# Optimization experiments

Hardware: AMD Instinct MI355X
Metric: run time of the kernel (lower is better)

## Reference

```python
import jax, jax.numpy as jnp
import numpy as np

N, K, SD, ID, ZD, ED, H, FC, AT, FT = 10000, 31, 8, 2, 32, 64, 128, 128, 16, 6
DT = 0.25


def setup_inputs() -> dict:
    key = jax.random.key(0)
    ks = iter(jax.random.split(key, 48))

    def p(shape, s=0.08):
        return (s * jax.random.normal(next(ks), shape)).astype(jnp.float32)

    E = N * K
    inp = {
        'state_history': p([4, N, SD], 1.0),          # only last slice is used
        'z': p([N, ZD], 1.0),                         # latent code per node
        'edge_idx1': jnp.repeat(jnp.arange(N), K),    # owning node of each edge
        'edge_idx2': jax.random.randint(next(ks), [E], 0, N),  # neighbor node
        'node_obs_idx': 1 + jnp.arange(E).reshape(N, K),  # +1: row 0 of enc table is the zero-pad row
        'W_edge': p([2 * SD, ED]), 'b_edge': jnp.zeros([ED], jnp.float32),
        'att_W1': p([ED, AT]), 'att_W2': p([SD, AT]), 'att_v': p([AT]),
        'obs_Wi': p([ED, 4 * H]), 'obs_Wh': p([H, 4 * H]), 'obs_b': jnp.zeros([4 * H], jnp.float32),
        'st_Wi': p([SD + ID, 4 * H]), 'st_Wh': p([H, 4 * H]), 'st_b': jnp.zeros([4 * H], jnp.float32),
        'oh0_W': p([SD, H]), 'oh0_b': jnp.zeros([H], jnp.float32),
        'oc0_W': p([SD, H]), 'oc0_b': jnp.zeros([H], jnp.float32),
        'sh0_W': p([SD, H]), 'sh0_b': jnp.zeros([H], jnp.float32),
        'sc0_W': p([SD, H]), 'sc0_b': jnp.zeros([H], jnp.float32),
        'act_W1': p([SD + H + H + ZD, FC]), 'act_b1': jnp.zeros([FC], jnp.float32),
        'act_W2': p([FC, ID]), 'act_b2': jnp.zeros([ID], jnp.float32),
        'dyn_A': p([SD, SD]), 'dyn_B': p([SD, ID]),
        'ft': FT,
    }
    return inp


def _lstm_step(x, h, c, Wi, Wh, b):
    g = x @ Wi + h @ Wh + b
    i, f, gg, o = jnp.split(g, 4, axis=-1)  # torch gate order i,f,g,o
    c2 = jax.nn.sigmoid(f) * c + jax.nn.sigmoid(i) * jnp.tanh(gg)
    h2 = jax.nn.sigmoid(o) * jnp.tanh(c2)
    return h2, c2


def reference(state_history, z, edge_idx1, edge_idx2, node_obs_idx,
              W_edge, b_edge, att_W1, att_W2, att_v,
              obs_Wi, obs_Wh, obs_b, st_Wi, st_Wh, st_b,
              oh0_W, oh0_b, oc0_W, oc0_b, sh0_W, sh0_b, sc0_W, sc0_b,
              act_W1, act_b1, act_W2, act_b2, dyn_A, dyn_B, ft):
    s0 = state_history[-1]                      # [N, SD]
    oh = s0 @ oh0_W + oh0_b                     # LSTM initial states from last history state
    oc = s0 @ oc0_W + oc0_b
    sh = s0 @ sh0_W + sh0_b
    sc = s0 @ sc0_W + sc0_b
    u0 = jnp.zeros((s0.shape[0], dyn_B.shape[1]), s0.dtype)

    def step(carry, _):
        s, u, oh, oc, sh, sc = carry
        # heterogeneous edge encoding: gather endpoint states, encode
        e = jnp.concatenate([s[edge_idx1], s[edge_idx2]], axis=-1)   # [E, 2*SD]
        enc = jax.nn.relu(e @ W_edge + b_edge)                       # [E, ED]
        enc_pad = jnp.concatenate([jnp.zeros((1, enc.shape[1]), enc.dtype), enc], axis=0)
        obs = enc_pad[node_obs_idx]                                  # [N, K, ED] gather
        rel = s - s0                                                  # rel_state_fun
        # additive attention over each node's K observed edges
        score = jnp.einsum('nki,i->nk', jnp.tanh(obs @ att_W1 + (rel @ att_W2)[:, None, :]), att_v)
        alpha = jax.nn.softmax(score, axis=-1)
        ctx = jnp.einsum('nk,nke->ne', alpha, obs)                   # [N, ED]
        oh2, oc2 = _lstm_step(ctx, oh, oc, obs_Wi, obs_Wh, obs_b)
        sh2, sc2 = _lstm_step(jnp.concatenate([rel, u], axis=-1), sh, sc, st_Wi, st_Wh, st_b)
        a = jnp.concatenate([rel, oh2, sh2, z], axis=-1)             # [N, SD+2H+ZD]
        u2 = jax.nn.relu(a @ act_W1 + act_b1) @ act_W2 + act_b2      # action net (input_scale=1)
        s2 = s + DT * (s @ dyn_A.T + u2 @ dyn_B.T)                   # dyn_net rollout
        return (s2, u2, oh2, oc2, sh2, sc2), (s2, u2)

    _, (state_pred, input_pred) = jax.lax.scan(step, (s0, u0, oh, oc, sh, sc), None, length=ft)
    return state_pred, input_pred  # [ft, N, SD], [ft, N, ID]
```

## Files before the change

kernel.cpp:

```cpp
#include <hip/hip_runtime.h>
#include <hip/hip_bf16.h>
#include <math.h>

#define N_NODES 10000
#define KE 31
#define SD 8
#define ID 2
#define ZD 32
#define ED 64
#define HH 128
#define FC 128
#define AT 16
#define FT 6
#define DT_C 0.25f
#define NB 4

#define NTU 20
#define MT 2

#define NKS_O 6
#define NKS_S 5
#define NKS_A 10

#define WP_OBS_SZ 49152
#define WP_ST_SZ  40960
#define WP_ACT_SZ 20480
#define WP_EDGE_SZ 1024
#define WP_ATT1_SZ 512

typedef __bf16 bf16x8 __attribute__((ext_vector_type(8)));
typedef float  f32x4  __attribute__((ext_vector_type(4)));

__device__ __forceinline__ float sigm(float x){ return 1.0f/(1.0f+exp2f(-1.44269504f*x)); }
__device__ __forceinline__ float tanh_f(float x){ return 1.0f - 2.0f/(1.0f+exp2f(2.88539008f*x)); }

__device__ __forceinline__ unsigned short f2b(float f){
  __hip_bfloat16 h = __float2bfloat16(f);
  return __builtin_bit_cast(unsigned short, h);
}
__device__ __forceinline__ float b2f(unsigned short x){
  unsigned int u = ((unsigned int)x) << 16;
  return __builtin_bit_cast(float, u);
}
__device__ __forceinline__ unsigned int pack2(float a, float b){
  return (unsigned int)f2b(a) | ((unsigned int)f2b(b) << 16);
}
__device__ __forceinline__ bf16x8 as_bf16x8(int4 v){
  union { int4 i; bf16x8 b; } u; u.i = v; return u.b;
}
__device__ __forceinline__ int hwaddr(int e, int d){
  return e*64 + ((((d>>3)<<3) ^ ((e&7)<<3)) + (d&7));
}

__global__ __launch_bounds__(256) void pack_weights(
    const float* __restrict__ obs_Wi, const float* __restrict__ obs_Wh,
    const float* __restrict__ st_Wi,  const float* __restrict__ st_Wh,
    const float* __restrict__ act_W1, const float* __restrict__ W_edge,
    const float* __restrict__ att_W1,
    unsigned int* __restrict__ wp_obs, unsigned int* __restrict__ wp_st,
    unsigned int* __restrict__ wp_act, unsigned int* __restrict__ wp_edge,
    unsigned int* __restrict__ wp_att1)
{
  int t = blockIdx.x*256 + threadIdx.x;
  if (t < 49152){
    int c = t / 1536; int r = t - c*1536;
    int ks = r >> 8; int q = r & 255;
    int ln = q >> 2; int dw = q & 3;
    int k  = ks*32 + ((ln>>4)<<3) + dw*2;
    int col = (c<<4) + (ln & 15);
    float v0 = (k   < 64) ? obs_Wi[k*4*HH + col]      : obs_Wh[(k-64)*4*HH + col];
    float v1 = (k+1 < 64) ? obs_Wi[(k+1)*4*HH + col]  : obs_Wh[(k-63)*4*HH + col];
    wp_obs[t] = pack2(v0, v1);
  } else if (t < 90112){
    int t2 = t - 49152;
    int c = t2 / 1280; int r = t2 - c*1280;
    int ks = r >> 8; int q = r & 255;
    int ln = q >> 2; int dw = q & 3;
    int k  = ks*32 + ((ln>>4)<<3) + dw*2;
    int col = (c<<4) + (ln & 15);
    float v0, v1;
    { int kk=k;   v0 = (kk<10)? st_Wi[kk*4*HH+col] : (kk<138 ? st_Wh[(kk-10)*4*HH+col] : 0.f); }
    { int kk=k+1; v1 = (kk<10)? st_Wi[kk*4*HH+col] : (kk<138 ? st_Wh[(kk-10)*4*HH+col] : 0.f); }
    wp_st[t2] = pack2(v0, v1);
  } else if (t < 110592){
    int t3 = t - 90112;
    int c = t3 / 2560; int r = t3 - c*2560;
    int ks = r >> 8; int q = r & 255;
    int ln = q >> 2; int dw = q & 3;
    int k  = ks*32 + ((ln>>4)<<3) + dw*2;
    int col = (c<<4) + (ln & 15);
    float v0 = (k   < 296) ? act_W1[k*FC + col]     : 0.f;
    float v1 = (k+1 < 296) ? act_W1[(k+1)*FC + col] : 0.f;
    wp_act[t3] = pack2(v0, v1);
  } else if (t < 111616){
    int t4 = t - 110592;
    int c = t4 >> 8; int r = t4 & 255;
    int ln = r >> 2; int dw = r & 3;
    int k  = ((ln>>4)<<3) + dw*2;
    int col = (c<<4) + (ln & 15);
    float v0 = (k   < 16) ? W_edge[k*ED + col]     : 0.f;
    float v1 = (k+1 < 16) ? W_edge[(k+1)*ED + col] : 0.f;
    wp_edge[t4] = pack2(v0, v1);
  } else if (t < 112128){
    int t5 = t - 111616;
    int ks = t5 >> 8; int r = t5 & 255;
    int ln = r >> 2; int dw = r & 3;
    int k  = ks*32 + ((ln>>4)<<3) + dw*2;
    int col = ln & 15;
    float v0 = (k   < 64) ? att_W1[k*AT + col]     : 0.f;
    float v1 = (k+1 < 64) ? att_W1[(k+1)*AT + col] : 0.f;
    wp_att1[t5] = pack2(v0, v1);
  }
}

__global__ __launch_bounds__(256) void init_kernel(
    const float* __restrict__ s0,
    const float* __restrict__ oh0_W, const float* __restrict__ oh0_b,
    const float* __restrict__ oc0_W, const float* __restrict__ oc0_b,
    const float* __restrict__ sh0_W, const float* __restrict__ sh0_b,
    const float* __restrict__ sc0_W, const float* __restrict__ sc0_b,
    unsigned short* __restrict__ oh, unsigned short* __restrict__ oc,
    unsigned short* __restrict__ sh, unsigned short* __restrict__ sc,
    float* __restrict__ u, unsigned short* __restrict__ s0bf)
{
  int t = blockIdx.x*256 + threadIdx.x;
  if (t < N_NODES*ID) u[t] = 0.0f;
  if (t < N_NODES*SD) s0bf[t] = f2b(s0[t]);
  if (t >= N_NODES*HH) return;
  int n = t >> 7, j = t & 127;
  float s[SD];
  #pragma unroll
  for (int i=0;i<SD;i++) s[i] = s0[n*SD+i];
  float a0=oh0_b[j], a1=oc0_b[j], a2=sh0_b[j], a3=sc0_b[j];
  #pragma unroll
  for (int i=0;i<SD;i++){
    a0 = fmaf(s[i], oh0_W[i*HH+j], a0);
    a1 = fmaf(s[i], oc0_W[i*HH+j], a1);
    a2 = fmaf(s[i], sh0_W[i*HH+j], a2);
    a3 = fmaf(s[i], sc0_W[i*HH+j], a3);
  }
  oh[t]=f2b(a0); oc[t]=f2b(a1); sh[t]=f2b(a2); sc[t]=f2b(a3);
}

__global__ __launch_bounds__(256) void edge_att_mfma(
    const float* __restrict__ s_prev, const float* __restrict__ s0,
    const unsigned short* __restrict__ sprev_bf,
    const int* __restrict__ edge_idx1, const int* __restrict__ edge_idx2,
    const int* __restrict__ node_obs_idx,
    const unsigned int* __restrict__ wp_edge, const unsigned int* __restrict__ wp_att1,
    const float* __restrict__ b_edge, const float* __restrict__ att_W2,
    const float* __restrict__ att_v, unsigned short* __restrict__ ctx)
{
  __shared__ __align__(16) unsigned int eF[8*64*4];
  __shared__ __align__(16) unsigned short encL[128*64];
  __shared__ __align__(16) unsigned int pF[4*64*4];
  __shared__ float scores[128];
  __shared__ float relbuf[NB][SD];
  __shared__ float relW2b[NB][AT];
  __shared__ unsigned char emask[128];

  const int tid  = threadIdx.x;
  const int lane = tid & 63;
  const int w    = tid >> 6;
  const int n0   = blockIdx.x * NB;
  const int EPB  = NB*KE;

  {
    ((uint4*)pF)[tid] = (uint4){0,0,0,0};
    int eb  = tid >> 1;
    int khi = tid & 1;
    int valid = 0;
    uint4 d = (uint4){0,0,0,0};
    if (eb < EPB){
      int nl = eb / KE;
      int j  = eb - nl*KE;
      int idx = node_obs_idx[(n0+nl)*KE + j];
      if (idx > 0){
        valid = 1;
        int e = idx - 1;
        int i = khi ? edge_idx2[e] : edge_idx1[e];
        d = *(const uint4*)&sprev_bf[i*SD];
      }
    }
    int mt = eb >> 4;
    int base = ((mt<<6) + (eb&15) + (khi<<4)) << 2;
    ((uint4*)&eF[base])[0] = d;
    int zbase = ((mt<<6) + (eb&15) + ((khi+2)<<4)) << 2;
    ((uint4*)&eF[zbase])[0] = (uint4){0,0,0,0};
    if (khi == 0) emask[eb] = (unsigned char)valid;
    if (tid < NB*SD){
      int m = tid >> 3, i = tid & 7;
      relbuf[m][i] = s_prev[(n0+m)*SD + i] - s0[(n0+m)*SD + i];
    }
  }
  __syncthreads();

  if (tid < NB*AT){
    int m = tid >> 4, a = tid & 15;
    float acc = 0.f;
    #pragma unroll
    for (int i = 0; i < SD; ++i) acc = fmaf(relbuf[m][i], att_W2[i*AT + a], acc);
    relW2b[m][a] = acc;
  }
  {
    const int c = lane & 15, g = lane >> 4;
    #pragma unroll
    for (int q = 0; q < 2; ++q){
      int mt = w*2 + q;
      bf16x8 A = as_bf16x8(*(const int4*)&eF[((mt<<6) + lane) << 2]);
      f32x4 acc[4];
      #pragma unroll
      for (int ct = 0; ct < 4; ++ct){
        bf16x8 B = as_bf16x8(*(const int4*)&wp_edge[((ct<<6) + lane) << 2]);
        acc[ct] = (f32x4){0,0,0,0};
        acc[ct] = __builtin_amdgcn_mfma_f32_16x16x32_bf16(A, B, acc[ct], 0, 0, 0);
      }
      #pragma unroll
      for (int ct = 0; ct < 4; ++ct){
        int d = ct*16 + c;
        float bias = b_edge[d];
        #pragma unroll
        for (int r = 0; r < 4; ++r){
          int eb = mt*16 + g*4 + r;
          float v = acc[ct][r] + bias;
          v = emask[eb] ? fmaxf(v, 0.f) : 0.f;
          encL[hwaddr(eb, d)] = f2b(v);
        }
      }
    }
  }
  __syncthreads();

  {
    const int c = lane & 15, g = lane >> 4;
    const float av = att_v[c];
    #pragma unroll
    for (int q = 0; q < 2; ++q){
      int mt = w*2 + q;
      int row = mt*16 + c;
      f32x4 acc = (f32x4){0,0,0,0};
      #pragma unroll
      for (int ks = 0; ks < 2; ++ks){
        int hw = row*64 + (((ks*4 + g) << 3) ^ ((row&7) << 3));
        bf16x8 A = *(const bf16x8*)&encL[hw];
        bf16x8 B = as_bf16x8(*(const int4*)&wp_att1[((ks<<6) + lane) << 2]);
        acc = __builtin_amdgcn_mfma_f32_16x16x32_bf16(A, B, acc, 0, 0, 0);
      }
      #pragma unroll
      for (int r = 0; r < 4; ++r){
        int eb = mt*16 + g*4 + r;
        int nm = eb / KE; if (nm > NB-1) nm = NB-1;
        float sv = av * tanh_f(acc[r] + relW2b[nm][c]);
        #pragma unroll
        for (int off = 1; off < 16; off <<= 1) sv += __shfl_xor(sv, off);
        if (c == 0 && eb < EPB) scores[eb] = sv;
      }
    }
  }
  __syncthreads();

  {
    int m = w;
    float sc_ = (lane < KE) ? scores[m*KE + lane] : -INFINITY;
    float mx = sc_;
    #pragma unroll
    for (int off = 32; off; off >>= 1) mx = fmaxf(mx, __shfl_xor(mx, off));
    float p = (lane < KE) ? exp2f(1.44269504f*(sc_ - mx)) : 0.f;
    float sm = p;
    #pragma unroll
    for (int off = 32; off; off >>= 1) sm += __shfl_xor(sm, off);
    float alpha = p / sm;
    if (lane < KE){
      int k = m*KE + lane;
      int ks = k >> 5;
      int ln = m | (((k>>3)&3) << 4);
      ((unsigned short*)pF)[((ks<<6) + ln)*8 + (k&7)] = f2b(alpha);
    }
  }
  __syncthreads();

  {
    const int c = lane & 15, g = lane >> 4;
    const int d = w*16 + c;
    f32x4 acc = (f32x4){0,0,0,0};
    #pragma unroll
    for (int ks = 0; ks < 4; ++ks){
      bf16x8 A = as_bf16x8(*(const int4*)&pF[((ks<<6) + lane) << 2]);
      union { unsigned short u[8]; bf16x8 v; } bb;
      #pragma unroll
      for (int j = 0; j < 8; ++j){
        int e = ks*32 + g*8 + j;
        bb.u[j] = encL[hwaddr(e, d)];
      }
      acc = __builtin_amdgcn_mfma_f32_16x16x32_bf16(A, bb.v, acc, 0, 0, 0);
    }
    if (g == 0){
      #pragma unroll
      for (int r = 0; r < 4; ++r){
        ctx[(n0 + r)*ED + d] = f2b(acc[r]);
      }
    }
  }
}

__global__ __launch_bounds__(512) void node_update_mfma(
    const float* __restrict__ s_prev, const float* __restrict__ s0,
    const float* __restrict__ z, const unsigned short* __restrict__ ctx,
    const unsigned int* __restrict__ wp_obs, const unsigned int* __restrict__ wp_st,
    const unsigned int* __restrict__ wp_act,
    const float* __restrict__ obs_b, const float* __restrict__ st_b,
    const float* __restrict__ act_b1,
    const float* __restrict__ act_W2, const float* __restrict__ act_b2,
    const float* __restrict__ dyn_A, const float* __restrict__ dyn_B,
    unsigned short* __restrict__ oh, unsigned short* __restrict__ oc,
    unsigned short* __restrict__ sh, unsigned short* __restrict__ sc,
    float* __restrict__ u, float* __restrict__ s_next,
    unsigned short* __restrict__ snext_bf,
    float* __restrict__ out_state, float* __restrict__ out_input, int tstep)
{
  __shared__ __align__(16) union UB {
    struct { unsigned int X1[MT*NKS_O*64*4]; unsigned int X2[MT*NKS_S*64*4]; } x;
    float F[32][FC+4];
  } ubuf;
  __shared__ __align__(16) unsigned int fragX3[MT*NKS_A*64*4];
  __shared__ float sps[32][SD];
  __shared__ float u2p[32][ID][4];
  __shared__ float u2s[32][ID];

  const int tid  = threadIdx.x;
  const int n0   = blockIdx.x * NTU;
  const int w    = tid >> 6;
  const int lane = tid & 63;
  const int hcol = w*16 + (lane & 15);

  float ocv[MT][4], scv[MT][4];
  #pragma unroll
  for (int Mt = 0; Mt < MT; ++Mt){
    #pragma unroll
    for (int r = 0; r < 4; ++r){
      int m = Mt*16 + ((lane>>4)<<2) + r;
      int gn = n0 + m;
      ocv[Mt][r] = (m < NTU) ? b2f(oc[gn*HH + hcol]) : 0.f;
      scv[Mt][r] = (m < NTU) ? b2f(sc[gn*HH + hcol]) : 0.f;
    }
  }

  for (int idx = tid; idx < 32*96; idx += 512){
    int m = idx / 96, kp = idx - m*96; int k0 = kp*2; int gn = n0 + m;
    unsigned int d = 0;
    if (m < NTU){
      if (k0 < ED) d = *(const unsigned int*)&ctx[gn*ED + k0];
      else         d = *(const unsigned int*)&oh[gn*HH + k0 - ED];
    }
    int Mt = m >> 4;
    int ln = (m & 15) | (((k0>>3)&3)<<4);
    ubuf.x.X1[(((Mt*NKS_O + (k0>>5))*64 + ln)<<2) + ((k0&7)>>1)] = d;
  }
  for (int idx = tid; idx < 32*80; idx += 512){
    int m = idx / 80, kp = idx - m*80; int k0 = kp*2; int gn = n0 + m;
    unsigned int d = 0;
    if (m < NTU){
      if (k0 < 8)        d = pack2(s_prev[gn*SD+k0]-s0[gn*SD+k0], s_prev[gn*SD+k0+1]-s0[gn*SD+k0+1]);
      else if (k0 == 8)  d = pack2(u[gn*ID], u[gn*ID+1]);
      else if (k0 < 138) d = *(const unsigned int*)&sh[gn*HH + k0 - 10];
    }
    int Mt = m >> 4;
    int ln = (m & 15) | (((k0>>3)&3)<<4);
    ubuf.x.X2[(((Mt*NKS_S + (k0>>5))*64 + ln)<<2) + ((k0&7)>>1)] = d;
  }
  for (int idx = tid; idx < 32*32; idx += 512){
    int m = idx / 32, p = idx - m*32; int gn = n0 + m;
    int k0 = (p < 4) ? p*2 : 256 + p*2;
    float v0 = 0.f, v1 = 0.f;
    if (m < NTU){
      if (k0 < 8){ v0 = s_prev[gn*SD+k0]-s0[gn*SD+k0]; v1 = s_prev[gn*SD+k0+1]-s0[gn*SD+k0+1]; }
      else if (k0 < 296){ v0 = z[gn*ZD + k0-264]; v1 = z[gn*ZD + k0-263]; }
    }
    int Mt = m >> 4;
    int ln = (m & 15) | (((k0>>3)&3)<<4);
    fragX3[(((Mt*NKS_A + (k0>>5))*64 + ln)<<2) + ((k0&7)>>1)] = pack2(v0, v1);
  }
  if (tid < NTU*SD){
    int m = tid >> 3, i = tid & 7;
    sps[m][i] = s_prev[(n0+m)*SD + i];
  }
  __syncthreads();

  {
    f32x4 acc[MT][4];
    #pragma unroll
    for (int Mt = 0; Mt < MT; ++Mt)
      #pragma unroll
      for (int g = 0; g < 4; ++g){
        float b = obs_b[g*HH + hcol];
        acc[Mt][g] = (f32x4){b, b, b, b};
      }
    #pragma unroll
    for (int ks = 0; ks < NKS_O; ++ks){
      bf16x8 a[MT];
      #pragma unroll
      for (int Mt = 0; Mt < MT; ++Mt)
        a[Mt] = as_bf16x8(*(const int4*)&ubuf.x.X1[(((Mt*NKS_O + ks)*64 + lane)<<2)]);
      #pragma unroll
      for (int g = 0; g < 4; ++g){
        int c = w + 8*g;
        bf16x8 b = as_bf16x8(*(const int4*)&wp_obs[(((c*NKS_O + ks)*64 + lane)<<2)]);
        #pragma unroll
        for (int Mt = 0; Mt < MT; ++Mt)
          acc[Mt][g] = __builtin_amdgcn_mfma_f32_16x16x32_bf16(a[Mt], b, acc[Mt][g], 0, 0, 0);
      }
    }
    #pragma unroll
    for (int Mt = 0; Mt < MT; ++Mt){
      #pragma unroll
      for (int r = 0; r < 4; ++r){
        int m = Mt*16 + ((lane>>4)<<2) + r; int gn = n0 + m;
        float h2 = 0.f;
        if (m < NTU){
          float gi = acc[Mt][0][r], gf = acc[Mt][1][r], gg = acc[Mt][2][r], go = acc[Mt][3][r];
          float c2 = sigm(gf)*ocv[Mt][r] + sigm(gi)*tanh_f(gg);
          h2 = sigm(go)*tanh_f(c2);
          oc[gn*HH + hcol] = f2b(c2);
          oh[gn*HH + hcol] = f2b(h2);
        }
        int k = 8 + hcol;
        int ln = (m & 15) | (((k>>3)&3)<<4);
        ((unsigned short*)fragX3)[(((m>>4)*NKS_A + (k>>5))*64 + ln)*8 + (k&7)] = f2b(h2);
      }
    }
  }

  {
    f32x4 acc[MT][4];
    #pragma unroll
    for (int Mt = 0; Mt < MT; ++Mt)
      #pragma unroll
      for (int g = 0; g < 4; ++g){
        float b = st_b[g*HH + hcol];
        acc[Mt][g] = (f32x4){b, b, b, b};
      }
    #pragma unroll
    for (int ks = 0; ks < NKS_S; ++ks){
      bf16x8 a[MT];
      #pragma unroll
      for (int Mt = 0; Mt < MT; ++Mt)
        a[Mt] = as_bf16x8(*(const int4*)&ubuf.x.X2[(((Mt*NKS_S + ks)*64 + lane)<<2)]);
      #pragma unroll
      for (int g = 0; g < 4; ++g){
        int c = w + 8*g;
        bf16x8 b = as_bf16x8(*(const int4*)&wp_st[(((c*NKS_S + ks)*64 + lane)<<2)]);
        #pragma unroll
        for (int Mt = 0; Mt < MT; ++Mt)
          acc[Mt][g] = __builtin_amdgcn_mfma_f32_16x16x32_bf16(a[Mt], b, acc[Mt][g], 0, 0, 0);
      }
    }
    #pragma unroll
    for (int Mt = 0; Mt < MT; ++Mt){
      #pragma unroll
      for (int r = 0; r < 4; ++r){
        int m = Mt*16 + ((lane>>4)<<2) + r; int gn = n0 + m;
        float h2 = 0.f;
        if (m < NTU){
          float gi = acc[Mt][0][r], gf = acc[Mt][1][r], gg = acc[Mt][2][r], go = acc[Mt][3][r];
          float c2 = sigm(gf)*scv[Mt][r] + sigm(gi)*tanh_f(gg);
          h2 = sigm(go)*tanh_f(c2);
          sc[gn*HH + hcol] = f2b(c2);
          sh[gn*HH + hcol] = f2b(h2);
        }
        int k = 136 + hcol;
        int ln = (m & 15) | (((k>>3)&3)<<4);
        ((unsigned short*)fragX3)[(((m>>4)*NKS_A + (k>>5))*64 + ln)*8 + (k&7)] = f2b(h2);
      }
    }
  }
  __syncthreads();

  {
    float b1 = act_b1[hcol];
    f32x4 acc[MT];
    #pragma unroll
    for (int Mt = 0; Mt < MT; ++Mt) acc[Mt] = (f32x4){b1, b1, b1, b1};
    #pragma unroll
    for (int ks = 0; ks < NKS_A; ++ks){
      bf16x8 bb = as_bf16x8(*(const int4*)&wp_act[(((w*NKS_A + ks)*64 + lane)<<2)]);
      #pragma unroll
      for (int Mt = 0; Mt < MT; ++Mt){
        bf16x8 a = as_bf16x8(*(const int4*)&fragX3[(((Mt*NKS_A + ks)*64 + lane)<<2)]);
        acc[Mt] = __builtin_amdgcn_mfma_f32_16x16x32_bf16(a, bb, acc[Mt], 0, 0, 0);
      }
    }
    #pragma unroll
    for (int Mt = 0; Mt < MT; ++Mt){
      #pragma unroll
      for (int r = 0; r < 4; ++r){
        int m = Mt*16 + ((lane>>4)<<2) + r;
        ubuf.F[m][hcol] = fmaxf(acc[Mt][r], 0.f);
      }
    }
  }
  __syncthreads();

  if (tid < 32*ID*4){
    int m  = tid >> 3;
    int c  = (tid >> 2) & 1;
    int kq = tid & 3;
    float p = 0.f;
    #pragma unroll
    for (int i = 0; i < 32; ++i){
      int j = kq*32 + i;
      p = fmaf(ubuf.F[m][j], act_W2[j*ID + c], p);
    }
    u2p[m][c][kq] = p;
  }
  __syncthreads();
  if (tid < NTU*ID){
    int m = tid >> 1, c = tid & 1; int gn = n0 + m;
    float s = act_b2[c] + u2p[m][c][0] + u2p[m][c][1] + u2p[m][c][2] + u2p[m][c][3];
    u2s[m][c] = s;
    u[gn*ID + c] = s;
    out_input[tstep*N_NODES*ID + gn*ID + c] = s;
  }
  __syncthreads();

  if (tid < NTU*SD){
    int m = tid >> 3, d = tid & 7; int gn = n0 + m;
    float acc = 0.f;
    #pragma unroll
    for (int e = 0; e < SD; ++e) acc = fmaf(sps[m][e], dyn_A[d*SD+e], acc);
    #pragma unroll
    for (int c = 0; c < ID; ++c) acc = fmaf(u2s[m][c], dyn_B[d*ID+c], acc);
    float s2v = sps[m][d] + DT_C*acc;
    s_next[gn*SD+d] = s2v;
    snext_bf[gn*SD+d] = f2b(s2v);
    out_state[tstep*N_NODES*SD + gn*SD + d] = s2v;
  }
}

extern "C" void kernel_launch(void* const* d_in, const int* in_sizes, int n_in,
                              void* d_out, int out_size, void* d_ws, size_t ws_size,
                              hipStream_t stream)
{
  const float* state_history = (const float*)d_in[0];
  const float* z        = (const float*)d_in[1];
  const int*   edge_idx1 = (const int*)d_in[2];
  const int*   edge_idx2 = (const int*)d_in[3];
  const int*   node_obs_idx = (const int*)d_in[4];
  const float* W_edge  = (const float*)d_in[5];
  const float* b_edge  = (const float*)d_in[6];
  const float* att_W1  = (const float*)d_in[7];
  const float* att_W2  = (const float*)d_in[8];
  const float* att_v   = (const float*)d_in[9];
  const float* obs_Wi  = (const float*)d_in[10];
  const float* obs_Wh  = (const float*)d_in[11];
  const float* obs_b   = (const float*)d_in[12];
  const float* st_Wi   = (const float*)d_in[13];
  const float* st_Wh   = (const float*)d_in[14];
  const float* st_b    = (const float*)d_in[15];
  const float* oh0_W   = (const float*)d_in[16];
  const float* oh0_b   = (const float*)d_in[17];
  const float* oc0_W   = (const float*)d_in[18];
  const float* oc0_b   = (const float*)d_in[19];
  const float* sh0_W   = (const float*)d_in[20];
  const float* sh0_b   = (const float*)d_in[21];
  const float* sc0_W   = (const float*)d_in[22];
  const float* sc0_b   = (const float*)d_in[23];
  const float* act_W1  = (const float*)d_in[24];
  const float* act_b1  = (const float*)d_in[25];
  const float* act_W2  = (const float*)d_in[26];
  const float* act_b2  = (const float*)d_in[27];
  const float* dyn_A   = (const float*)d_in[28];
  const float* dyn_B   = (const float*)d_in[29];

  const float* s0 = state_history + 3*N_NODES*SD;

  float* wsf = (float*)d_ws;
  float* sbuf0 = wsf;
  float* sbuf1 = sbuf0 + N_NODES*SD;
  float* u     = sbuf1 + N_NODES*SD;
  unsigned short* oh    = (unsigned short*)(u + N_NODES*ID);
  unsigned short* oc    = oh + N_NODES*HH;
  unsigned short* sh    = oc + N_NODES*HH;
  unsigned short* sc    = sh + N_NODES*HH;
  unsigned short* ctx   = sc + N_NODES*HH;
  unsigned short* s0bf  = ctx + N_NODES*ED;
  unsigned short* sbf0  = s0bf + N_NODES*SD;
  unsigned short* sbf1  = sbf0 + N_NODES*SD;
  float* sbuf[2] = { sbuf0, sbuf1 };
  unsigned short* sbf[2] = { sbf0, sbf1 };

  unsigned int* wp_obs  = (unsigned int*)(sbf1 + N_NODES*SD);
  unsigned int* wp_st   = wp_obs + WP_OBS_SZ;
  unsigned int* wp_act  = wp_st  + WP_ST_SZ;
  unsigned int* wp_edge = wp_act + WP_ACT_SZ;
  unsigned int* wp_att1 = wp_edge + WP_EDGE_SZ;

  float* out_state = (float*)d_out;
  float* out_input = out_state + FT*N_NODES*SD;

  hipLaunchKernelGGL(pack_weights, dim3(438), dim3(256), 0, stream,
      obs_Wi, obs_Wh, st_Wi, st_Wh, act_W1, W_edge, att_W1,
      wp_obs, wp_st, wp_act, wp_edge, wp_att1);

  hipLaunchKernelGGL(init_kernel, dim3((N_NODES*HH+255)/256), dim3(256), 0, stream,
      s0, oh0_W, oh0_b, oc0_W, oc0_b, sh0_W, sh0_b, sc0_W, sc0_b, oh, oc, sh, sc, u, s0bf);

  for (int t = 0; t < FT; ++t){
    const float* s_prev = (t==0) ? s0 : sbuf[(t-1)&1];
    const unsigned short* sprev_bf = (t==0) ? s0bf : sbf[(t-1)&1];
    float* s_next = sbuf[t&1];
    unsigned short* snext_bf = sbf[t&1];
    hipLaunchKernelGGL(edge_att_mfma, dim3(N_NODES/NB), dim3(256), 0, stream,
        s_prev, s0, sprev_bf, edge_idx1, edge_idx2, node_obs_idx,
        wp_edge, wp_att1, b_edge, att_W2, att_v, ctx);
    hipLaunchKernelGGL(node_update_mfma, dim3(N_NODES/NTU), dim3(512), 0, stream,
        s_prev, s0, z, ctx,
        wp_obs, wp_st, wp_act,
        obs_b, st_b, act_b1, act_W2, act_b2, dyn_A, dyn_B,
        oh, oc, sh, sc, u, s_next, snext_bf, out_state, out_input, t);
  }
}
```

Baseline: 310.0 us.

## Fill full 32-row MFMA tiles per block and split row tiles across 16 waves

The node update kernel now assigns 32 real nodes per block instead of 20, so the two 16-row MFMA tiles carry no padding rows. It also doubles the block to 1024 threads, giving each wave a single row tile (Mth) and a column tile (ct), so the gate and action GEMMs are spread over twice as many waves. A tail guard (nreal) handles the last partial block. The goal is less wasted MFMA work on padding and more parallelism per block. The cost is fewer blocks, larger register and LDS pressure per block, and repeated weight fragment loads across the two row-tile waves.

Measured after the change: 358.9 us. 1.16x slower.

```diff
diff --git a/kernel.cpp b/kernel.cpp
--- a/kernel.cpp
+++ b/kernel.cpp
@@ -15,7 +15,7 @@
 #define DT_C 0.25f
 #define NB 4
 
-#define NTU 20
+#define NTU 32
 #define MT 2
 
 #define NKS_O 6
@@ -303,7 +303,7 @@
   }
 }
 
-__global__ __launch_bounds__(512) void node_update_mfma(
+__global__ __launch_bounds__(1024) void node_update_mfma(
     const float* __restrict__ s_prev, const float* __restrict__ s0,
     const float* __restrict__ z, const unsigned short* __restrict__ ctx,
     const unsigned int* __restrict__ wp_obs, const unsigned int* __restrict__ wp_st,
@@ -329,26 +329,26 @@
 
   const int tid  = threadIdx.x;
   const int n0   = blockIdx.x * NTU;
+  const int nreal= (N_NODES - n0 < NTU) ? (N_NODES - n0) : NTU;
   const int w    = tid >> 6;
+  const int ct   = w & 7;
+  const int Mth  = w >> 3;
   const int lane = tid & 63;
-  const int hcol = w*16 + (lane & 15);
-
-  float ocv[MT][4], scv[MT][4];
+  const int hcol = ct*16 + (lane & 15);
+
+  float ocv[4], scv[4];
   #pragma unroll
-  for (int Mt = 0; Mt < MT; ++Mt){
-    #pragma unroll
-    for (int r = 0; r < 4; ++r){
-      int m = Mt*16 + ((lane>>4)<<2) + r;
-      int gn = n0 + m;
-      ocv[Mt][r] = (m < NTU) ? b2f(oc[gn*HH + hcol]) : 0.f;
-      scv[Mt][r] = (m < NTU) ? b2f(sc[gn*HH + hcol]) : 0.f;
-    }
-  }
-
-  for (int idx = tid; idx < 32*96; idx += 512){
+  for (int r = 0; r < 4; ++r){
+    int m = Mth*16 + ((lane>>4)<<2) + r;
+    int gn = n0 + m;
+    ocv[r] = (m < nreal) ? b2f(oc[gn*HH + hcol]) : 0.f;
+    scv[r] = (m < nreal) ? b2f(sc[gn*HH + hcol]) : 0.f;
+  }
+
+  for (int idx = tid; idx < 32*96; idx += 1024){
     int m = idx / 96, kp = idx - m*96; int k0 = kp*2; int gn = n0 + m;
     unsigned int d = 0;
-    if (m < NTU){
+    if (m < nreal){
       if (k0 < ED) d = *(const unsigned int*)&ctx[gn*ED + k0];
       else         d = *(const unsigned int*)&oh[gn*HH + k0 - ED];
     }
@@ -356,10 +356,10 @@
     int ln = (m & 15) | (((k0>>3)&3)<<4);
     ubuf.x.X1[(((Mt*NKS_O + (k0>>5))*64 + ln)<<2) + ((k0&7)>>1)] = d;
   }
-  for (int idx = tid; idx < 32*80; idx += 512){
+  for (int idx = tid; idx < 32*80; idx += 1024){
     int m = idx / 80, kp = idx - m*80; int k0 = kp*2; int gn = n0 + m;
     unsigned int d = 0;
-    if (m < NTU){
+    if (m < nreal){
       if (k0 < 8)        d = pack2(s_prev[gn*SD+k0]-s0[gn*SD+k0], s_prev[gn*SD+k0+1]-s0[gn*SD+k0+1]);
       else if (k0 == 8)  d = pack2(u[gn*ID], u[gn*ID+1]);
       else if (k0 < 138) d = *(const unsigned int*)&sh[gn*HH + k0 - 10];
@@ -368,11 +368,11 @@
     int ln = (m & 15) | (((k0>>3)&3)<<4);
     ubuf.x.X2[(((Mt*NKS_S + (k0>>5))*64 + ln)<<2) + ((k0&7)>>1)] = d;
   }
-  for (int idx = tid; idx < 32*32; idx += 512){
+  for (int idx = tid; idx < 32*32; idx += 1024){
     int m = idx / 32, p = idx - m*32; int gn = n0 + m;
     int k0 = (p < 4) ? p*2 : 256 + p*2;
     float v0 = 0.f, v1 = 0.f;
-    if (m < NTU){
+    if (m < nreal){
       if (k0 < 8){ v0 = s_prev[gn*SD+k0]-s0[gn*SD+k0]; v1 = s_prev[gn*SD+k0+1]-s0[gn*SD+k0+1]; }
       else if (k0 < 296){ v0 = z[gn*ZD + k0-264]; v1 = z[gn*ZD + k0-263]; }
     }
@@ -382,120 +382,92 @@
   }
   if (tid < NTU*SD){
     int m = tid >> 3, i = tid & 7;
-    sps[m][i] = s_prev[(n0+m)*SD + i];
-  }
-  __syncthreads();
-
-  {
-    f32x4 acc[MT][4];
-    #pragma unroll
-    for (int Mt = 0; Mt < MT; ++Mt)
+    sps[m][i] = (m < nreal) ? s_prev[(n0+m)*SD + i] : 0.f;
+  }
+  __syncthreads();
+
+  {
+    f32x4 acc[4];
+    #pragma unroll
+    for (int g = 0; g < 4; ++g){
+      float b = obs_b[g*HH + hcol];
+      acc[g] = (f32x4){b, b, b, b};
+    }
+    #pragma unroll
+    for (int ks = 0; ks < NKS_O; ++ks){
+      bf16x8 a = as_bf16x8(*(const int4*)&ubuf.x.X1[(((Mth*NKS_O + ks)*64 + lane)<<2)]);
       #pragma unroll
       for (int g = 0; g < 4; ++g){
-        float b = obs_b[g*HH + hcol];
-        acc[Mt][g] = (f32x4){b, b, b, b};
-      }
-    #pragma unroll
-    for (int ks = 0; ks < NKS_O; ++ks){
-      bf16x8 a[MT];
-      #pragma unroll
-      for (int Mt = 0; Mt < MT; ++Mt)
-        a[Mt] = as_bf16x8(*(const int4*)&ubuf.x.X1[(((Mt*NKS_O + ks)*64 + lane)<<2)]);
+        int c = ct + 8*g;
+        bf16x8 b = as_bf16x8(*(const int4*)&wp_obs[(((c*NKS_O + ks)*64 + lane)<<2)]);
+        acc[g] = __builtin_amdgcn_mfma_f32_16x16x32_bf16(a, b, acc[g], 0, 0, 0);
+      }
+    }
+    #pragma unroll
+    for (int r = 0; r < 4; ++r){
+      int m = Mth*16 + ((lane>>4)<<2) + r; int gn = n0 + m;
+      float h2 = 0.f;
+      if (m < nreal){
+        float gi = acc[0][r], gf = acc[1][r], gg = acc[2][r], go = acc[3][r];
+        float c2 = sigm(gf)*ocv[r] + sigm(gi)*tanh_f(gg);
+        h2 = sigm(go)*tanh_f(c2);
+        oc[gn*HH + hcol] = f2b(c2);
+        oh[gn*HH + hcol] = f2b(h2);
+      }
+      int k = 8 + hcol;
+      int ln = (m & 15) | (((k>>3)&3)<<4);
+      ((unsigned short*)fragX3)[(((m>>4)*NKS_A + (k>>5))*64 + ln)*8 + (k&7)] = f2b(h2);
+    }
+  }
+
+  {
+    f32x4 acc[4];
+    #pragma unroll
+    for (int g = 0; g < 4; ++g){
+      float b = st_b[g*HH + hcol];
+      acc[g] = (f32x4){b, b, b, b};
+    }
+    #pragma unroll
+    for (int ks = 0; ks < NKS_S; ++ks){
+      bf16x8 a = as_bf16x8(*(const int4*)&ubuf.x.X2[(((Mth*NKS_S + ks)*64 + lane)<<2)]);
       #pragma unroll
       for (int g = 0; g < 4; ++g){
-        int c = w + 8*g;
-        bf16x8 b = as_bf16x8(*(const int4*)&wp_obs[(((c*NKS_O + ks)*64 + lane)<<2)]);
-        #pragma unroll
-        for (int Mt = 0; Mt < MT; ++Mt)
-          acc[Mt][g] = __builtin_amdgcn_mfma_f32_16x16x32_bf16(a[Mt], b, acc[Mt][g], 0, 0, 0);
-      }
-    }
-    #pragma unroll
-    for (int Mt = 0; Mt < MT; ++Mt){
-      #pragma unroll
-      for (int r = 0; r < 4; ++r){
-        int m = Mt*16 + ((lane>>4)<<2) + r; int gn = n0 + m;
-        float h2 = 0.f;
-        if (m < NTU){
-          float gi = acc[Mt][0][r], gf = acc[Mt][1][r], gg = acc[Mt][2][r], go = acc[Mt][3][r];
-          float c2 = sigm(gf)*ocv[Mt][r] + sigm(gi)*tanh_f(gg);
-          h2 = sigm(go)*tanh_f(c2);
-          oc[gn*HH + hcol] = f2b(c2);
-          oh[gn*HH + hcol] = f2b(h2);
-        }
-        int k = 8 + hcol;
-        int ln = (m & 15) | (((k>>3)&3)<<4);
-        ((unsigned short*)fragX3)[(((m>>4)*NKS_A + (k>>5))*64 + ln)*8 + (k&7)] = f2b(h2);
-      }
-    }
-  }
-
-  {
-    f32x4 acc[MT][4];
-    #pragma unroll
-    for (int Mt = 0; Mt < MT; ++Mt)
-      #pragma unroll
-      for (int g = 0; g < 4; ++g){
-        float b = st_b[g*HH + hcol];
-        acc[Mt][g] = (f32x4){b, b, b, b};
-      }
-    #pragma unroll
-    for (int ks = 0; ks < NKS_S; ++ks){
-      bf16x8 a[MT];
-      #pragma unroll
-      for (int Mt = 0; Mt < MT; ++Mt)
-        a[Mt] = as_bf16x8(*(const int4*)&ubuf.x.X2[(((Mt*NKS_S + ks)*64 + lane)<<2)]);
-      #pragma unroll
-      for (int g = 0; g < 4; ++g){
-        int c = w + 8*g;
+        int c = ct + 8*g;
         bf16x8 b = as_bf16x8(*(const int4*)&wp_st[(((c*NKS_S + ks)*64 + lane)<<2)]);
-        #pragma unroll
-        for (int Mt = 0; Mt < MT; ++Mt)
-          acc[Mt][g] = __builtin_amdgcn_mfma_f32_16x16x32_bf16(a[Mt], b, acc[Mt][g], 0, 0, 0);
-      }
-    }
-    #pragma unroll
-    for (int Mt = 0; Mt < MT; ++Mt){
-      #pragma unroll
-      for (int r = 0; r < 4; ++r){
-        int m = Mt*16 + ((lane>>4)<<2) + r; int gn = n0 + m;
-        float h2 = 0.f;
-        if (m < NTU){
-          float gi = acc[Mt][0][r], gf = acc[Mt][1][r], gg = acc[Mt][2][r], go = acc[Mt][3][r];
-          float c2 = sigm(gf)*scv[Mt][r] + sigm(gi)*tanh_f(gg);
-          h2 = sigm(go)*tanh_f(c2);
-          sc[gn*HH + hcol] = f2b(c2);
-          sh[gn*HH + hcol] = f2b(h2);
-        }
-        int k = 136 + hcol;
-        int ln = (m & 15) | (((k>>3)&3)<<4);
-        ((unsigned short*)fragX3)[(((m>>4)*NKS_A + (k>>5))*64 + ln)*8 + (k&7)] = f2b(h2);
-      }
+        acc[g] = __builtin_amdgcn_mfma_f32_16x16x32_bf16(a, b, acc[g], 0, 0, 0);
+      }
+    }
+    #pragma unroll
+    for (int r = 0; r < 4; ++r){
+      int m = Mth*16 + ((lane>>4)<<2) + r; int gn = n0 + m;
+      float h2 = 0.f;
+      if (m < nreal){
+        float gi = acc[0][r], gf = acc[1][r], gg = acc[2][r], go = acc[3][r];
+        float c2 = sigm(gf)*scv[r] + sigm(gi)*tanh_f(gg);
+        h2 = sigm(go)*tanh_f(c2);
+        sc[gn*HH + hcol] = f2b(c2);
+        sh[gn*HH + hcol] = f2b(h2);
+      }
+      int k = 136 + hcol;
+      int ln = (m & 15) | (((k>>3)&3)<<4);
+      ((unsigned short*)fragX3)[(((m>>4)*NKS_A + (k>>5))*64 + ln)*8 + (k&7)] = f2b(h2);
     }
   }
   __syncthreads();
 
   {
     float b1 = act_b1[hcol];
-    f32x4 acc[MT];
-    #pragma unroll
-    for (int Mt = 0; Mt < MT; ++Mt) acc[Mt] = (f32x4){b1, b1, b1, b1};
+    f32x4 acc = (f32x4){b1, b1, b1, b1};
     #pragma unroll
     for (int ks = 0; ks < NKS_A; ++ks){
-      bf16x8 bb = as_bf16x8(*(const int4*)&wp_act[(((w*NKS_A + ks)*64 + lane)<<2)]);
-      #pragma unroll
-      for (int Mt = 0; Mt < MT; ++Mt){
-        bf16x8 a = as_bf16x8(*(const int4*)&fragX3[(((Mt*NKS_A + ks)*64 + lane)<<2)]);
-        acc[Mt] = __builtin_amdgcn_mfma_f32_16x16x32_bf16(a, bb, acc[Mt], 0, 0, 0);
-      }
-    }
-    #pragma unroll
-    for (int Mt = 0; Mt < MT; ++Mt){
-      #pragma unroll
-      for (int r = 0; r < 4; ++r){
-        int m = Mt*16 + ((lane>>4)<<2) + r;
-        ubuf.F[m][hcol] = fmaxf(acc[Mt][r], 0.f);
-      }
+      bf16x8 bb = as_bf16x8(*(const int4*)&wp_act[(((ct*NKS_A + ks)*64 + lane)<<2)]);
+      bf16x8 a = as_bf16x8(*(const int4*)&fragX3[(((Mth*NKS_A + ks)*64 + lane)<<2)]);
+      acc = __builtin_amdgcn_mfma_f32_16x16x32_bf16(a, bb, acc, 0, 0, 0);
+    }
+    #pragma unroll
+    for (int r = 0; r < 4; ++r){
+      int m = Mth*16 + ((lane>>4)<<2) + r;
+      ubuf.F[m][hcol] = fmaxf(acc[r], 0.f);
     }
   }
   __syncthreads();
@@ -515,24 +487,28 @@
   __syncthreads();
   if (tid < NTU*ID){
     int m = tid >> 1, c = tid & 1; int gn = n0 + m;
-    float s = act_b2[c] + u2p[m][c][0] + u2p[m][c][1] + u2p[m][c][2] + u2p[m][c][3];
-    u2s[m][c] = s;
-    u[gn*ID + c] = s;
-    out_input[tstep*N_NODES*ID + gn*ID + c] = s;
+    if (m < nreal){
+      float s = act_b2[c] + u2p[m][c][0] + u2p[m][c][1] + u2p[m][c][2] + u2p[m][c][3];
+      u2s[m][c] = s;
+      u[gn*ID + c] = s;
+      out_input[tstep*N_NODES*ID + gn*ID + c] = s;
+    }
   }
   __syncthreads();
 
   if (tid < NTU*SD){
     int m = tid >> 3, d = tid & 7; int gn = n0 + m;
-    float acc = 0.f;
-    #pragma unroll
-    for (int e = 0; e < SD; ++e) acc = fmaf(sps[m][e], dyn_A[d*SD+e], acc);
-    #pragma unroll
-    for (int c = 0; c < ID; ++c) acc = fmaf(u2s[m][c], dyn_B[d*ID+c], acc);
-    float s2v = sps[m][d] + DT_C*acc;
-    s_next[gn*SD+d] = s2v;
-    snext_bf[gn*SD+d] = f2b(s2v);
-    out_state[tstep*N_NODES*SD + gn*SD + d] = s2v;
+    if (m < nreal){
+      float acc = 0.f;
+      #pragma unroll
+      for (int e = 0; e < SD; ++e) acc = fmaf(sps[m][e], dyn_A[d*SD+e], acc);
+      #pragma unroll
+      for (int c = 0; c < ID; ++c) acc = fmaf(u2s[m][c], dyn_B[d*ID+c], acc);
+      float s2v = sps[m][d] + DT_C*acc;
+      s_next[gn*SD+d] = s2v;
+      snext_bf[gn*SD+d] = f2b(s2v);
+      out_state[tstep*N_NODES*SD + gn*SD + d] = s2v;
+    }
   }
 }
 
@@ -604,6 +580,7 @@
   hipLaunchKernelGGL(init_kernel, dim3((N_NODES*HH+255)/256), dim3(256), 0, stream,
       s0, oh0_W, oh0_b, oc0_W, oc0_b, sh0_W, sh0_b, sc0_W, sc0_b, oh, oc, sh, sc, u, s0bf);
 
+  const int grid2 = (N_NODES + NTU - 1) / NTU;
   for (int t = 0; t < FT; ++t){
     const float* s_prev = (t==0) ? s0 : sbuf[(t-1)&1];
     const unsigned short* sprev_bf = (t==0) ? s0bf : sbf[(t-1)&1];
@@ -612,7 +589,7 @@
     hipLaunchKernelGGL(edge_att_mfma, dim3(N_NODES/NB), dim3(256), 0, stream,
         s_prev, s0, sprev_bf, edge_idx1, edge_idx2, node_obs_idx,
         wp_edge, wp_att1, b_edge, att_W2, att_v, ctx);
-    hipLaunchKernelGGL(node_update_mfma, dim3(N_NODES/NTU), dim3(512), 0, stream,
+    hipLaunchKernelGGL(node_update_mfma, dim3(grid2), dim3(1024), 0, stream,
         s_prev, s0, z, ctx,
         wp_obs, wp_st, wp_act,
         obs_b, st_b, act_b1, act_W2, act_b2, dyn_A, dyn_B,
```
